# Kernel optimization log

Measured on AMD Instinct MI355X. Metric: run time of the kernel, lower is better.

## Reference

```python
import jax, jax.numpy as jnp
import numpy as np

NUM_NODES = 4096
IN_DIM = 16
HIDDEN = 64
OUT_DIM = 32
HEADS = 4
NEG_SLOPE = 0.2
NEG_INF = -1e9


def _glorot(key, shape):
    fan_in, fan_out = shape[0], shape[-1]
    lim = jnp.sqrt(6.0 / (fan_in + fan_out))
    return jax.random.uniform(key, shape, jnp.float32, -lim, lim)


def setup_inputs() -> dict:
    key = jax.random.key(0)
    ks = jax.random.split(key, 8)
    B = 2
    return {
        "x": jax.random.normal(ks[0], (B, NUM_NODES, IN_DIM), jnp.float32),
        "embedding": _glorot(ks[1], (NUM_NODES, HIDDEN)),
        "W_proj": _glorot(ks[2], (IN_DIM, HIDDEN)),
        "b_proj": jnp.zeros((HIDDEN,), jnp.float32),
        "W1": _glorot(ks[3], (HIDDEN, HIDDEN)),  # heads=4, 16 per head, concat -> 64
        "att1_src": _glorot(ks[4], (HEADS, HIDDEN // HEADS)),
        "att1_dst": _glorot(ks[5], (HEADS, HIDDEN // HEADS)),
        "b1": jnp.zeros((HIDDEN,), jnp.float32),
        "W2": _glorot(ks[6], (HIDDEN, OUT_DIM)),  # heads=4, 8 per head, concat -> 32
        "att2_src": _glorot(ks[7], (HEADS, OUT_DIM // HEADS)),
        "att2_dst": _glorot(jax.random.fold_in(key, 99), (HEADS, OUT_DIM // HEADS)),
        "b2": jnp.zeros((OUT_DIM,), jnp.float32),
    }


def _gat(x, mask, W, a_src, a_dst, b):
    """Dense masked GAT layer. x: [B,N,Fin], mask: [N,N] bool (shared over batch).

    Equivalent to GATConv over edge list tf.where(adj > 0.5): for each target i,
    softmax over neighbors j of LeakyReLU(a_dst.Wh_i + a_src.Wh_j), aggregate Wh_j.
    """
    B, N, _ = x.shape
    H, F = a_src.shape
    h = (x @ W).reshape(B, N, H, F)                       # [B,N,H,F]
    s_src = jnp.einsum('bnhf,hf->bnh', h, a_src)          # per-source score
    s_dst = jnp.einsum('bnhf,hf->bnh', h, a_dst)          # per-target score
    e = s_dst[:, :, None, :] + s_src[:, None, :, :]       # [B,i,j,H]
    e = jnp.where(e > 0, e, NEG_SLOPE * e)                # LeakyReLU(0.2)
    e = jnp.where(mask[None, :, :, None], e, NEG_INF)
    alpha = jax.nn.softmax(e, axis=2)                     # softmax over neighbors j
    out = jnp.einsum('bijh,bjhf->bihf', alpha, h).reshape(B, N, H * F)
    return out + b


def reference(x, embedding, W_proj, b_proj, W1, att1_src, att1_dst, b1,
              W2, att2_src, att2_dst, b2):
    # AdaptiveAdjacency: cosine similarity of l2-normalized node embeddings
    ne = embedding / jnp.linalg.norm(embedding, axis=-1, keepdims=True)
    adj = ne @ ne.T                                       # [N,N], same for all batch
    mask = adj > 0.5                                      # edge set (incl. self-loops)

    h = x @ W_proj + b_proj                               # Dense proj -> hidden
    h = jax.nn.relu(_gat(h, mask, W1, att1_src, att1_dst, b1))
    return _gat(h, mask, W2, att2_src, att2_dst, b2)
```

## Files before the change

kernel.cpp:

```cpp
#include <hip/hip_runtime.h>
#include <hip/hip_bf16.h>
#include <stdint.h>

#define N_NODES 4096
#define BATCH 2

typedef __attribute__((ext_vector_type(8))) short short8v;
typedef __attribute__((ext_vector_type(4))) unsigned short ushort4v;
typedef __attribute__((ext_vector_type(4))) float f32x4;

#define GLL16(gsrc, ldst) \
    __builtin_amdgcn_global_load_lds((const __attribute__((address_space(1))) void*)(gsrc), \
                                     (__attribute__((address_space(3))) void*)(ldst), 16, 0, 0)

static __device__ inline unsigned short f2bf_rn(float x) {
    unsigned u = __float_as_uint(x);
    unsigned r = (u + 0x7FFFu + ((u >> 16) & 1u)) >> 16;
    return (unsigned short)r;
}
static __device__ inline float bf2f(unsigned short b) {
    return __uint_as_float(((unsigned)b) << 16);
}
static __device__ inline float rl(float v, int k) {
    return __uint_as_float(__builtin_amdgcn_readlane(__float_as_uint(v), k));
}

__global__ __launch_bounds__(256) void norm_kernel(
        const float* __restrict__ emb,
        unsigned short* __restrict__ ne_hi, unsigned short* __restrict__ ne_lo) {
    int t = threadIdx.x;
    int row = blockIdx.x * 16 + (t >> 4);
    int l16 = t & 15;
    float4 v = *(const float4*)&emb[(size_t)row * 64 + l16 * 4];
    float s = v.x * v.x + v.y * v.y + v.z * v.z + v.w * v.w;
#pragma unroll
    for (int m = 8; m >= 1; m >>= 1) s += __shfl_xor(s, m);
    float inv = 1.f / sqrtf(s);
    float n0 = v.x * inv, n1 = v.y * inv, n2 = v.z * inv, n3 = v.w * inv;
    ushort4v h = {f2bf_rn(n0), f2bf_rn(n1), f2bf_rn(n2), f2bf_rn(n3)};
    ushort4v lo = {f2bf_rn(n0 - bf2f(h.x)), f2bf_rn(n1 - bf2f(h.y)),
                   f2bf_rn(n2 - bf2f(h.z)), f2bf_rn(n3 - bf2f(h.w))};
    *(ushort4v*)&ne_hi[(size_t)row * 64 + l16 * 4] = h;
    *(ushort4v*)&ne_lo[(size_t)row * 64 + l16 * 4] = lo;
}

__global__ __launch_bounds__(256) void k2_kernel(
        const unsigned short* __restrict__ hi, const unsigned short* __restrict__ lo,
        unsigned long long* __restrict__ mask,
        const float* __restrict__ x, const float* __restrict__ Wp,
        const float* __restrict__ bp, const float* __restrict__ W1,
        const float* __restrict__ a1s, const float* __restrict__ a1d,
        float* __restrict__ h1out, float* __restrict__ ssrc, float* __restrict__ sdst) {
    __shared__ unsigned short Ah[128 * 64];
    __shared__ unsigned short Al[128 * 64];
    __shared__ unsigned short Bh[128 * 64];
    __shared__ unsigned short Bl[128 * 64];
    int t = threadIdx.x;
    int w = t >> 6, l = t & 63;

    if (blockIdx.x < 256) {
        int b = blockIdx.x;
        int row0 = b * 32 + w * 8;

        float xv[8];
#pragma unroll
        for (int r = 0; r < 8; ++r) xv[r] = x[(size_t)(row0 + r) * 16 + (l & 15)];

        float h0[8];
        float bpv = bp[l];
#pragma unroll
        for (int r = 0; r < 8; ++r) h0[r] = bpv;
#pragma unroll
        for (int k = 0; k < 16; ++k) {
            float wk = Wp[k * 64 + l];
#pragma unroll
            for (int r = 0; r < 8; ++r) h0[r] += rl(xv[r], k) * wk;
        }

        float h1[8] = {0.f, 0.f, 0.f, 0.f, 0.f, 0.f, 0.f, 0.f};
#pragma unroll
        for (int k = 0; k < 64; ++k) {
            float wk = W1[k * 64 + l];
#pragma unroll
            for (int r = 0; r < 8; ++r) h1[r] += rl(h0[r], k) * wk;
        }

        float as_ = a1s[l], ad_ = a1d[l];
#pragma unroll
        for (int r = 0; r < 8; ++r) {
            h1out[(size_t)(row0 + r) * 64 + l] = h1[r];
            float ps = h1[r] * as_, pd = h1[r] * ad_;
#pragma unroll
            for (int m = 8; m >= 1; m >>= 1) {
                ps += __shfl_xor(ps, m);
                pd += __shfl_xor(pd, m);
            }
            if ((l & 15) == 0) {
                ssrc[(size_t)(row0 + r) * 4 + (l >> 4)] = ps;
                sdst[(size_t)(row0 + r) * 4 + (l >> 4)] = pd;
            }
        }
        return;
    }

    int tile = blockIdx.x - 256;
    int bi = tile >> 5, bj = tile & 31;
    int i0 = bi * 128, j0 = bj * 128;

    int cr = l >> 3;
    int slot = (l & 7) ^ cr;
#pragma unroll
    for (int q = 0; q < 4; ++q) {
        int lr = w * 32 + q * 8;
        size_t ga = (size_t)(i0 + lr + cr) * 64 + slot * 8;
        size_t gb = (size_t)(j0 + lr + cr) * 64 + slot * 8;
        GLL16(hi + ga, &Ah[lr * 64]);
        GLL16(lo + ga, &Al[lr * 64]);
        GLL16(hi + gb, &Bh[lr * 64]);
        GLL16(lo + gb, &Bl[lr * 64]);
    }
    __syncthreads();

    int fr = l & 15;
    int s0 = l >> 4;
    int r7 = l & 7;
    short8v aH[2][2], aL[2][2];
#pragma unroll
    for (int rt = 0; rt < 2; ++rt) {
        int base = (w * 32 + rt * 16 + fr) * 64;
        aH[rt][0] = *(const short8v*)&Ah[base + ((s0 ^ r7) << 3)];
        aH[rt][1] = *(const short8v*)&Ah[base + (((s0 + 4) ^ r7) << 3)];
        aL[rt][0] = *(const short8v*)&Al[base + ((s0 ^ r7) << 3)];
        aL[rt][1] = *(const short8v*)&Al[base + (((s0 + 4) ^ r7) << 3)];
    }

    f32x4 acc[2][8];
#pragma unroll
    for (int rt = 0; rt < 2; ++rt)
#pragma unroll
        for (int js = 0; js < 8; ++js) acc[rt][js] = (f32x4){0.f, 0.f, 0.f, 0.f};

#pragma unroll
    for (int js = 0; js < 8; ++js) {
        int bbase = (js * 16 + fr) * 64;
        short8v bH0 = *(const short8v*)&Bh[bbase + ((s0 ^ r7) << 3)];
        short8v bH1 = *(const short8v*)&Bh[bbase + (((s0 + 4) ^ r7) << 3)];
        short8v bL0 = *(const short8v*)&Bl[bbase + ((s0 ^ r7) << 3)];
        short8v bL1 = *(const short8v*)&Bl[bbase + (((s0 + 4) ^ r7) << 3)];
#pragma unroll
        for (int rt = 0; rt < 2; ++rt) {
            f32x4 a = acc[rt][js];
            a = __builtin_amdgcn_mfma_f32_16x16x32_bf16(aH[rt][0], bH0, a, 0, 0, 0);
            a = __builtin_amdgcn_mfma_f32_16x16x32_bf16(aH[rt][1], bH1, a, 0, 0, 0);
            a = __builtin_amdgcn_mfma_f32_16x16x32_bf16(aH[rt][0], bL0, a, 0, 0, 0);
            a = __builtin_amdgcn_mfma_f32_16x16x32_bf16(aH[rt][1], bL1, a, 0, 0, 0);
            a = __builtin_amdgcn_mfma_f32_16x16x32_bf16(aL[rt][0], bH0, a, 0, 0, 0);
            a = __builtin_amdgcn_mfma_f32_16x16x32_bf16(aL[rt][1], bH1, a, 0, 0, 0);
            acc[rt][js] = a;
        }
    }

    int shift = ((l & 15) >> 2) * 16;
    int r = l & 3;
#pragma unroll
    for (int rt = 0; rt < 2; ++rt) {
#pragma unroll
        for (int ws_ = 0; ws_ < 2; ++ws_) {
            unsigned long long w64 = 0;
#pragma unroll
            for (int js2 = 0; js2 < 4; ++js2) {
                f32x4 a = acc[rt][ws_ * 4 + js2];
                unsigned long long c0 = __ballot(a[0] > 0.5f);
                unsigned long long c1 = __ballot(a[1] > 0.5f);
                unsigned long long c2 = __ballot(a[2] > 0.5f);
                unsigned long long c3 = __ballot(a[3] > 0.5f);
                unsigned long long sel = r == 0 ? c0 : r == 1 ? c1 : r == 2 ? c2 : c3;
                w64 |= ((sel >> shift) & 0xFFFFULL) << (js2 * 16);
            }
            if (l < 16)
                mask[(size_t)(i0 + w * 32 + rt * 16 + l) * 64 + bj * 2 + ws_] = w64;
        }
    }
}

__global__ __launch_bounds__(256) void agg1_fused_kernel(
        const float* __restrict__ h1, const float* __restrict__ ssrc,
        const float* __restrict__ sdst, const unsigned long long* __restrict__ mask,
        const float* __restrict__ b1, const float* __restrict__ W2,
        const float* __restrict__ a2s, const float* __restrict__ a2d,
        float* __restrict__ h2out, float* __restrict__ s2s, float* __restrict__ s2d) {
    int i = blockIdx.x * 4 + (threadIdx.x >> 6);
    int t = threadIdx.x & 63;
    int hh = t >> 4;

    float sdA = sdst[(size_t)i * 4 + hh];
    float sdB = sdst[(size_t)(i + N_NODES) * 4 + hh];
    unsigned long long myword = mask[(size_t)i * 64 + t];

    float mA = -1e30f, dA = 0.f, aA = 0.f;
    float mB = -1e30f, dB = 0.f, aB = 0.f;
    unsigned long long nz = __ballot(myword != 0ULL);
    while (nz) {
        int lw = __ffsll(nz) - 1;
        nz &= nz - 1;
        unsigned long long wbits = __shfl(myword, lw);
        while (wbits) {
            int bpos = __ffsll(wbits) - 1;
            wbits &= wbits - 1;
            int j = (lw << 6) + bpos;
            float ssA = ssrc[(size_t)j * 4 + hh];
            float ssB = ssrc[(size_t)(j + N_NODES) * 4 + hh];
            float hvA = h1[(size_t)j * 64 + t];
            float hvB = h1[(size_t)(j + N_NODES) * 64 + t];
            float e = sdA + ssA;
            e = e > 0.f ? e : 0.2f * e;
            float mn = fmaxf(mA, e);
            float cf = __expf(mA - mn);
            float wg = __expf(e - mn);
            dA = dA * cf + wg;
            aA = aA * cf + wg * hvA;
            mA = mn;
            e = sdB + ssB;
            e = e > 0.f ? e : 0.2f * e;
            mn = fmaxf(mB, e);
            cf = __expf(mB - mn);
            wg = __expf(e - mn);
            dB = dB * cf + wg;
            aB = aB * cf + wg * hvB;
            mB = mn;
        }
    }
    float b1v = b1[t];
    float oA = fmaxf(aA / dA + b1v, 0.f);
    float oB = fmaxf(aB / dB + b1v, 0.f);

    int l2 = t & 31;
    float acc2A = 0.f, acc2B = 0.f;
#pragma unroll
    for (int k = 0; k < 64; ++k) {
        float wk = W2[k * 32 + l2];
        acc2A += rl(oA, k) * wk;
        acc2B += rl(oB, k) * wk;
    }

    float a2sv = a2s[l2], a2dv = a2d[l2];
    float psA = acc2A * a2sv, pdA = acc2A * a2dv;
    float psB = acc2B * a2sv, pdB = acc2B * a2dv;
#pragma unroll
    for (int mm = 4; mm >= 1; mm >>= 1) {
        psA += __shfl_xor(psA, mm);
        pdA += __shfl_xor(pdA, mm);
        psB += __shfl_xor(psB, mm);
        pdB += __shfl_xor(pdB, mm);
    }
    if (t < 32) {
        h2out[(size_t)i * 32 + t] = acc2A;
        h2out[(size_t)(i + N_NODES) * 32 + t] = acc2B;
        if ((t & 7) == 0) {
            s2s[(size_t)i * 4 + (t >> 3)] = psA;
            s2d[(size_t)i * 4 + (t >> 3)] = pdA;
            s2s[(size_t)(i + N_NODES) * 4 + (t >> 3)] = psB;
            s2d[(size_t)(i + N_NODES) * 4 + (t >> 3)] = pdB;
        }
    }
}

__global__ __launch_bounds__(256) void agg2_kernel(
        const float* __restrict__ hfeat, const float* __restrict__ ssrc,
        const float* __restrict__ sdst, const unsigned long long* __restrict__ mask,
        const float* __restrict__ bias, float* __restrict__ out) {
    int i = blockIdx.x * 4 + (threadIdx.x >> 6);
    int t = threadIdx.x & 63;
    int tt = t & 31;
    int hh = tt >> 3;

    float sdA = sdst[(size_t)i * 4 + hh];
    float sdB = sdst[(size_t)(i + N_NODES) * 4 + hh];
    unsigned long long myword = mask[(size_t)i * 64 + t];

    float mA = -1e30f, dA = 0.f, aA = 0.f;
    float mB = -1e30f, dB = 0.f, aB = 0.f;
    unsigned long long nz = __ballot(myword != 0ULL);
    while (nz) {
        int lw = __ffsll(nz) - 1;
        nz &= nz - 1;
        unsigned long long wbits = __shfl(myword, lw);
        while (wbits) {
            int bpos = __ffsll(wbits) - 1;
            wbits &= wbits - 1;
            int j = (lw << 6) + bpos;
            float ssA = ssrc[(size_t)j * 4 + hh];
            float ssB = ssrc[(size_t)(j + N_NODES) * 4 + hh];
            float hvA = hfeat[(size_t)j * 32 + tt];
            float hvB = hfeat[(size_t)(j + N_NODES) * 32 + tt];
            float e = sdA + ssA;
            e = e > 0.f ? e : 0.2f * e;
            float mn = fmaxf(mA, e);
            float cf = __expf(mA - mn);
            float wg = __expf(e - mn);
            dA = dA * cf + wg;
            aA = aA * cf + wg * hvA;
            mA = mn;
            e = sdB + ssB;
            e = e > 0.f ? e : 0.2f * e;
            mn = fmaxf(mB, e);
            cf = __expf(mB - mn);
            wg = __expf(e - mn);
            dB = dB * cf + wg;
            aB = aB * cf + wg * hvB;
            mB = mn;
        }
    }
    float bv = bias[tt];
    if (t < 32) {
        out[(size_t)i * 32 + tt] = aA / dA + bv;
        out[(size_t)(i + N_NODES) * 32 + tt] = aB / dB + bv;
    }
}

extern "C" void kernel_launch(void* const* d_in, const int* in_sizes, int n_in,
                              void* d_out, int out_size, void* d_ws, size_t ws_size,
                              hipStream_t stream) {
    const float* x   = (const float*)d_in[0];
    const float* emb = (const float*)d_in[1];
    const float* Wp  = (const float*)d_in[2];
    const float* bp  = (const float*)d_in[3];
    const float* W1  = (const float*)d_in[4];
    const float* a1s = (const float*)d_in[5];
    const float* a1d = (const float*)d_in[6];
    const float* b1  = (const float*)d_in[7];
    const float* W2  = (const float*)d_in[8];
    const float* a2s = (const float*)d_in[9];
    const float* a2d = (const float*)d_in[10];
    const float* b2  = (const float*)d_in[11];

    const int ROWS = BATCH * N_NODES;

    char* w = (char*)d_ws;
    unsigned short* ne_hi = (unsigned short*)w;  w += (size_t)N_NODES * 64 * 2;
    unsigned short* ne_lo = (unsigned short*)w;  w += (size_t)N_NODES * 64 * 2;
    unsigned long long* mask = (unsigned long long*)w; w += (size_t)N_NODES * 64 * 8;
    float* h1  = (float*)w;                      w += (size_t)ROWS * 64 * 4;
    float* s1s = (float*)w;                      w += (size_t)ROWS * 4 * 4;
    float* s1d = (float*)w;                      w += (size_t)ROWS * 4 * 4;
    float* h2  = (float*)w;                      w += (size_t)ROWS * 32 * 4;
    float* s2s = (float*)w;                      w += (size_t)ROWS * 4 * 4;
    float* s2d = (float*)w;                      w += (size_t)ROWS * 4 * 4;

    norm_kernel<<<dim3(256), dim3(256), 0, stream>>>(emb, ne_hi, ne_lo);
    k2_kernel<<<dim3(1280), dim3(256), 0, stream>>>(
        ne_hi, ne_lo, mask, x, Wp, bp, W1, a1s, a1d, h1, s1s, s1d);
    agg1_fused_kernel<<<dim3(N_NODES / 4), dim3(256), 0, stream>>>(
        h1, s1s, s1d, mask, b1, W2, a2s, a2d, h2, s2s, s2d);
    agg2_kernel<<<dim3(N_NODES / 4), dim3(256), 0, stream>>>(
        h2, s2s, s2d, mask, b2, (float*)d_out);
}
```

Baseline: 34.20 us.

## Fuse embedding normalization into mask tile kernel via unnormalized dot threshold

Removes the separate norm kernel and the bf16 hi/lo workspace. Each mask tile now loads raw fp32 embeddings, splits them to bf16 hi/lo in registers and writes them to LDS, and computes per-row norms. The threshold becomes dot > 0.5·|a|·|b| rather than normalizing first. This saves one launch and a global round trip, but every tile redoes the conversion and norms for 256 rows from fp32 loads, which doubles the load bytes and replaces the async global-to-LDS copies. Rounding now applies to unnormalized values, which could flip borderline mask bits.

```diff
diff --git a/kernel.cpp b/kernel.cpp
--- a/kernel.cpp
+++ b/kernel.cpp
@@ -6,18 +6,8 @@
 #define BATCH 2
 
 typedef __attribute__((ext_vector_type(8))) short short8v;
-typedef __attribute__((ext_vector_type(4))) unsigned short ushort4v;
 typedef __attribute__((ext_vector_type(4))) float f32x4;
 
-#define GLL16(gsrc, ldst) \
-    __builtin_amdgcn_global_load_lds((const __attribute__((address_space(1))) void*)(gsrc), \
-                                     (__attribute__((address_space(3))) void*)(ldst), 16, 0, 0)
-
-static __device__ inline unsigned short f2bf_rn(float x) {
-    unsigned u = __float_as_uint(x);
-    unsigned r = (u + 0x7FFFu + ((u >> 16) & 1u)) >> 16;
-    return (unsigned short)r;
-}
 static __device__ inline float bf2f(unsigned short b) {
     return __uint_as_float(((unsigned)b) << 16);
 }
@@ -25,28 +15,24 @@
     return __uint_as_float(__builtin_amdgcn_readlane(__float_as_uint(v), k));
 }
 
-__global__ __launch_bounds__(256) void norm_kernel(
-        const float* __restrict__ emb,
-        unsigned short* __restrict__ ne_hi, unsigned short* __restrict__ ne_lo) {
-    int t = threadIdx.x;
-    int row = blockIdx.x * 16 + (t >> 4);
-    int l16 = t & 15;
-    float4 v = *(const float4*)&emb[(size_t)row * 64 + l16 * 4];
-    float s = v.x * v.x + v.y * v.y + v.z * v.z + v.w * v.w;
-#pragma unroll
-    for (int m = 8; m >= 1; m >>= 1) s += __shfl_xor(s, m);
-    float inv = 1.f / sqrtf(s);
-    float n0 = v.x * inv, n1 = v.y * inv, n2 = v.z * inv, n3 = v.w * inv;
-    ushort4v h = {f2bf_rn(n0), f2bf_rn(n1), f2bf_rn(n2), f2bf_rn(n3)};
-    ushort4v lo = {f2bf_rn(n0 - bf2f(h.x)), f2bf_rn(n1 - bf2f(h.y)),
-                   f2bf_rn(n2 - bf2f(h.z)), f2bf_rn(n3 - bf2f(h.w))};
-    *(ushort4v*)&ne_hi[(size_t)row * 64 + l16 * 4] = h;
-    *(ushort4v*)&ne_lo[(size_t)row * 64 + l16 * 4] = lo;
+static __device__ inline void cvt2(float f0, float f1, unsigned* hi, unsigned* lo) {
+    float2 p;
+    p.x = f0;
+    p.y = f1;
+    __hip_bfloat162 h = __float22bfloat162_rn(p);
+    unsigned hb;
+    __builtin_memcpy(&hb, &h, 4);
+    p.x = f0 - bf2f((unsigned short)hb);
+    p.y = f1 - bf2f((unsigned short)(hb >> 16));
+    __hip_bfloat162 l2v = __float22bfloat162_rn(p);
+    unsigned lb;
+    __builtin_memcpy(&lb, &l2v, 4);
+    *hi = hb;
+    *lo = lb;
 }
 
 __global__ __launch_bounds__(256) void k2_kernel(
-        const unsigned short* __restrict__ hi, const unsigned short* __restrict__ lo,
-        unsigned long long* __restrict__ mask,
+        const float* __restrict__ emb, unsigned long long* __restrict__ mask,
         const float* __restrict__ x, const float* __restrict__ Wp,
         const float* __restrict__ bp, const float* __restrict__ W1,
         const float* __restrict__ a1s, const float* __restrict__ a1d,
@@ -55,6 +41,8 @@
     __shared__ unsigned short Al[128 * 64];
     __shared__ unsigned short Bh[128 * 64];
     __shared__ unsigned short Bl[128 * 64];
+    __shared__ float An[128];
+    __shared__ float Bn[128];
     int t = threadIdx.x;
     int w = t >> 6, l = t & 63;
 
@@ -107,17 +95,49 @@
     int bi = tile >> 5, bj = tile & 31;
     int i0 = bi * 128, j0 = bj * 128;
 
-    int cr = l >> 3;
-    int slot = (l & 7) ^ cr;
-#pragma unroll
-    for (int q = 0; q < 4; ++q) {
-        int lr = w * 32 + q * 8;
-        size_t ga = (size_t)(i0 + lr + cr) * 64 + slot * 8;
-        size_t gb = (size_t)(j0 + lr + cr) * 64 + slot * 8;
-        GLL16(hi + ga, &Ah[lr * 64]);
-        GLL16(lo + ga, &Al[lr * 64]);
-        GLL16(hi + gb, &Bh[lr * 64]);
-        GLL16(lo + gb, &Bl[lr * 64]);
+    {
+        int rhalf = l >> 1, half = l & 1;
+        int row = w * 32 + rhalf;
+        float na = 0.f, nb = 0.f;
+#pragma unroll
+        for (int q = 0; q < 4; ++q) {
+            int slot = half * 4 + q;
+            const float* pa = &emb[(size_t)(i0 + row) * 64 + slot * 8];
+            const float* pb = &emb[(size_t)(j0 + row) * 64 + slot * 8];
+            float4 a0 = *(const float4*)pa;
+            float4 a1 = *(const float4*)(pa + 4);
+            float4 b0 = *(const float4*)pb;
+            float4 b1 = *(const float4*)(pb + 4);
+            na += a0.x * a0.x + a0.y * a0.y + a0.z * a0.z + a0.w * a0.w +
+                  a1.x * a1.x + a1.y * a1.y + a1.z * a1.z + a1.w * a1.w;
+            nb += b0.x * b0.x + b0.y * b0.y + b0.z * b0.z + b0.w * b0.w +
+                  b1.x * b1.x + b1.y * b1.y + b1.z * b1.z + b1.w * b1.w;
+
+            union {
+                unsigned u[4];
+                short8v v;
+            } HA, LA, HB, LB;
+            cvt2(a0.x, a0.y, &HA.u[0], &LA.u[0]);
+            cvt2(a0.z, a0.w, &HA.u[1], &LA.u[1]);
+            cvt2(a1.x, a1.y, &HA.u[2], &LA.u[2]);
+            cvt2(a1.z, a1.w, &HA.u[3], &LA.u[3]);
+            cvt2(b0.x, b0.y, &HB.u[0], &LB.u[0]);
+            cvt2(b0.z, b0.w, &HB.u[1], &LB.u[1]);
+            cvt2(b1.x, b1.y, &HB.u[2], &LB.u[2]);
+            cvt2(b1.z, b1.w, &HB.u[3], &LB.u[3]);
+
+            int ss = ((slot ^ (row & 7)) << 3);
+            *(short8v*)&Ah[row * 64 + ss] = HA.v;
+            *(short8v*)&Al[row * 64 + ss] = LA.v;
+            *(short8v*)&Bh[row * 64 + ss] = HB.v;
+            *(short8v*)&Bl[row * 64 + ss] = LB.v;
+        }
+        na += __shfl_xor(na, 1);
+        nb += __shfl_xor(nb, 1);
+        if (half == 0) {
+            An[row] = sqrtf(na);
+            Bn[row] = sqrtf(nb);
+        }
     }
     __syncthreads();
 
@@ -164,16 +184,23 @@
     int r = l & 3;
 #pragma unroll
     for (int rt = 0; rt < 2; ++rt) {
+        int rb = w * 32 + rt * 16 + (l >> 4) * 4;
+        float n0 = 0.5f * An[rb + 0];
+        float n1 = 0.5f * An[rb + 1];
+        float n2 = 0.5f * An[rb + 2];
+        float n3 = 0.5f * An[rb + 3];
 #pragma unroll
         for (int ws_ = 0; ws_ < 2; ++ws_) {
             unsigned long long w64 = 0;
 #pragma unroll
             for (int js2 = 0; js2 < 4; ++js2) {
-                f32x4 a = acc[rt][ws_ * 4 + js2];
-                unsigned long long c0 = __ballot(a[0] > 0.5f);
-                unsigned long long c1 = __ballot(a[1] > 0.5f);
-                unsigned long long c2 = __ballot(a[2] > 0.5f);
-                unsigned long long c3 = __ballot(a[3] > 0.5f);
+                int js = ws_ * 4 + js2;
+                float nbv = Bn[js * 16 + (l & 15)];
+                f32x4 a = acc[rt][js];
+                unsigned long long c0 = __ballot(a[0] > n0 * nbv);
+                unsigned long long c1 = __ballot(a[1] > n1 * nbv);
+                unsigned long long c2 = __ballot(a[2] > n2 * nbv);
+                unsigned long long c3 = __ballot(a[3] > n3 * nbv);
                 unsigned long long sel = r == 0 ? c0 : r == 1 ? c1 : r == 2 ? c2 : c3;
                 w64 |= ((sel >> shift) & 0xFFFFULL) << (js2 * 16);
             }
@@ -337,8 +364,6 @@
     const int ROWS = BATCH * N_NODES;
 
     char* w = (char*)d_ws;
-    unsigned short* ne_hi = (unsigned short*)w;  w += (size_t)N_NODES * 64 * 2;
-    unsigned short* ne_lo = (unsigned short*)w;  w += (size_t)N_NODES * 64 * 2;
     unsigned long long* mask = (unsigned long long*)w; w += (size_t)N_NODES * 64 * 8;
     float* h1  = (float*)w;                      w += (size_t)ROWS * 64 * 4;
     float* s1s = (float*)w;                      w += (size_t)ROWS * 4 * 4;
@@ -347,9 +372,8 @@
     float* s2s = (float*)w;                      w += (size_t)ROWS * 4 * 4;
     float* s2d = (float*)w;                      w += (size_t)ROWS * 4 * 4;
 
-    norm_kernel<<<dim3(256), dim3(256), 0, stream>>>(emb, ne_hi, ne_lo);
     k2_kernel<<<dim3(1280), dim3(256), 0, stream>>>(
-        ne_hi, ne_lo, mask, x, Wp, bp, W1, a1s, a1d, h1, s1s, s1d);
+        emb, mask, x, Wp, bp, W1, a1s, a1d, h1, s1s, s1d);
     agg1_fused_kernel<<<dim3(N_NODES / 4), dim3(256), 0, stream>>>(
         h1, s1s, s1d, mask, b1, W2, a2s, a2d, h2, s2s, s2d);
     agg2_kernel<<<dim3(N_NODES / 4), dim3(256), 0, stream>>>(
```

Measured after the change: 33.69 us. No clear change (-1.5%).
